# Performance work log

Hardware: AMD Instinct MI355X
Metric: run time of the kernel (lower is better)

The kernel has to match this reference:

```python
import jax, jax.numpy as jnp
import numpy as np

E, H, I = 8, 2048, 768  # num_experts, hidden_size, moe_intermediate_size
B, S = 4, 1024


def setup_inputs() -> dict:
    key = jax.random.key(0)
    k1, k2, k3, k4, k5 = jax.random.split(key, 5)
    hidden_states = jax.random.normal(k1, (B, S, H), dtype=jnp.float32)
    routing_weights = jax.random.uniform(k2, (B * S, E), dtype=jnp.float32)
    router_indices = jax.random.randint(k3, (B * S, 2), 0, E)
    gate_up_proj = jax.random.normal(k4, (E, H, 2 * I), dtype=jnp.float32) * 0.02
    down_proj = jax.random.normal(k5, (E, I, H), dtype=jnp.float32) * 0.02
    return {
        "hidden_states": hidden_states,
        "routing_weights": routing_weights,
        "router_indices": router_indices,
        "gate_up_proj": gate_up_proj,
        "down_proj": down_proj,
    }


def reference(hidden_states, routing_weights, router_indices, gate_up_proj, down_proj):
    b, s, h = hidden_states.shape
    x = hidden_states.reshape(-1, h)  # [T, H], T = B*S
    # dense all-experts: every token through every expert
    gate_up = jnp.einsum("th,ehd->etd", x, gate_up_proj)  # [E, T, 2I]
    gate, up = jnp.split(gate_up, 2, axis=-1)
    inter = up * jax.nn.silu(gate)  # [E, T, I]
    out = jnp.einsum("eti,eih->eth", inter, down_proj)  # [E, T, H]
    rw = routing_weights.T.reshape(out.shape[0], b, s)  # [E, B, S]
    out = out.reshape(out.shape[0], b, s, h) * rw[..., None]
    return out.sum(axis=0)  # [B, S, H]
```

## Files before the change

kernel.cpp:

```cpp
#include <hip/hip_runtime.h>
#include <cstdint>
#include <cstddef>

#define NE 8
#define NH 2048
#define NI 768
#define NT 4096
#define NK2 6144

typedef __bf16 bf16x8 __attribute__((ext_vector_type(8)));
typedef float f32x4 __attribute__((ext_vector_type(4)));
typedef unsigned short u16x8 __attribute__((ext_vector_type(8)));

__device__ __forceinline__ unsigned short f2bf(float f) {
  unsigned int u = __builtin_bit_cast(unsigned int, f);
  u += 0x7fffu + ((u >> 16) & 1u);
  return (unsigned short)(u >> 16);
}

__device__ __forceinline__ void gload_lds16(const void* g, void* s) {
  __builtin_amdgcn_global_load_lds(
      (const __attribute__((address_space(1))) unsigned int*)g,
      (__attribute__((address_space(3))) unsigned int*)s, 16, 0, 0);
}

__global__ __launch_bounds__(256) void k_cvt(const float* __restrict__ in,
                                             unsigned short* __restrict__ out,
                                             long n) {
  long i = ((long)blockIdx.x * blockDim.x + threadIdx.x) * 8;
  if (i >= n) return;
  float4 f0 = *reinterpret_cast<const float4*>(in + i);
  float4 f1 = *reinterpret_cast<const float4*>(in + i + 4);
  u16x8 o;
  o[0] = f2bf(f0.x); o[1] = f2bf(f0.y); o[2] = f2bf(f0.z); o[3] = f2bf(f0.w);
  o[4] = f2bf(f1.x); o[5] = f2bf(f1.y); o[6] = f2bf(f1.z); o[7] = f2bf(f1.w);
  *reinterpret_cast<u16x8*>(out + i) = o;
}

__global__ __launch_bounds__(256) void k_transpose_cvt(
    const float* __restrict__ in, unsigned short* __restrict__ out,
    int R, int C, long inBS, long outBS, int outCS, int mode) {
  __shared__ float tile[32][33];
  const int b = blockIdx.z;
  const int r0 = blockIdx.y * 32, c0 = blockIdx.x * 32;
  const int tx = threadIdx.x, ty = threadIdx.y;
  const float* ib = in + (long)b * inBS;
#pragma unroll
  for (int d = 0; d < 4; d++)
    tile[ty + d * 8][tx] = ib[(long)(r0 + ty + d * 8) * C + c0 + tx];
  __syncthreads();
#pragma unroll
  for (int d = 0; d < 4; d++) {
    int c = c0 + ty + d * 8;
    int r = r0 + tx;
    int orow;
    if (mode == 1) {
      int z = (c >= NI) ? 1 : 0;
      int cc = c - z * NI;
      orow = ((cc >> 4) << 5) + (z << 4) + (cc & 15);
    } else {
      orow = c;
    }
    out[(long)b * outBS + (long)orow * outCS + r] = f2bf(tile[tx][ty + d * 8]);
  }
}


__global__ __launch_bounds__(512, 1) void k_gemm1(
    const unsigned short* __restrict__ Xb,
    const unsigned short* __restrict__ W1t,
    const float* __restrict__ rw,
    unsigned short* __restrict__ inter) {
  __shared__ unsigned short ldsA[2][16384];
  __shared__ unsigned short ldsB[2][16384];

  const int e = blockIdx.z;
  const int t0 = blockIdx.y * 256;
  const int bn = blockIdx.x;
  const int tid = threadIdx.x;
  const int lane = tid & 63, wave = tid >> 6;
  const int wr = wave >> 2, wc = wave & 3;
  const int fr = lane & 15, fq = lane >> 4;
  const int nkt = NH / 64;

  const unsigned short* Bg = W1t + (size_t)e * (2 * NI) * NH;
  const int rih = tid >> 3, ck = tid & 7;
  const unsigned short* sA = Xb + (size_t)(t0 + rih) * NH + ((ck ^ (rih & 7)) << 3);
  const unsigned short* sB = Bg + (size_t)(bn * 256 + rih) * NH + ((ck ^ (rih & 7)) << 3);
  const int dst = tid * 8;

#define STG_H0(C) do { \
    const int cc_ = (C); const size_t ko_ = (size_t)cc_ * 64; \
    unsigned short* da_ = &ldsA[cc_ & 1][dst]; \
    unsigned short* db_ = &ldsB[cc_ & 1][dst]; \
    gload_lds16(sB + ko_, db_); \
    gload_lds16(sB + ko_ + (size_t)(64 * NH), db_ + 4096); \
    gload_lds16(sA + ko_, da_); \
    gload_lds16(sA + ko_ + (size_t)(64 * NH), da_ + 4096); \
  } while (0)
#define STG_H1(C) do { \
    const int cc_ = (C); const size_t ko_ = (size_t)cc_ * 64; \
    unsigned short* da_ = &ldsA[cc_ & 1][dst]; \
    unsigned short* db_ = &ldsB[cc_ & 1][dst]; \
    gload_lds16(sB + ko_ + (size_t)2 * (64 * NH), db_ + 8192); \
    gload_lds16(sB + ko_ + (size_t)3 * (64 * NH), db_ + 12288); \
    gload_lds16(sA + ko_ + (size_t)2 * (64 * NH), da_ + 8192); \
    gload_lds16(sA + ko_ + (size_t)3 * (64 * NH), da_ + 12288); \
  } while (0)
#define WAITV4 asm volatile("s_waitcnt vmcnt(4)" ::: "memory")
#define BAR do { __builtin_amdgcn_sched_barrier(0); \
                 __builtin_amdgcn_s_barrier(); \
                 __builtin_amdgcn_sched_barrier(0); } while (0)

  f32x4 acc[8][4];
#pragma unroll
  for (int i = 0; i < 8; ++i)
#pragma unroll
    for (int j = 0; j < 4; ++j) acc[i][j] = (f32x4){0.f, 0.f, 0.f, 0.f};

  const int swz = fr & 7;
  int aoff[8], boff[4];
#pragma unroll
  for (int i = 0; i < 8; ++i)
    aoff[i] = ((i >> 2) * 128 + wr * 64 + (i & 3) * 16 + fr) * 64 + ((fq ^ swz) << 3);
#pragma unroll
  for (int j = 0; j < 4; ++j)
    boff[j] = ((j >> 1) * 128 + wc * 32 + (j & 1) * 16 + fr) * 64 + ((fq ^ swz) << 3);
  const int dk = ((((4 + fq) ^ swz) - (fq ^ swz)) << 3);

  STG_H0(0);
  STG_H1(0);
  WAITV4;
  BAR;

  for (int kt = 0; kt < nkt; ++kt) {
    const int cur = kt & 1;
    const int nx = (kt + 1 < nkt) ? kt + 1 : nkt - 1;
    const unsigned short* lA = ldsA[cur];
    const unsigned short* lB = ldsB[cur];
    bf16x8 af0[4][2], af1[4][2], bf0[2][2], bf1[2][2];

#pragma unroll
    for (int m = 0; m < 4; ++m) {
      af0[m][0] = *reinterpret_cast<const bf16x8*>(lA + aoff[m]);
      af0[m][1] = *reinterpret_cast<const bf16x8*>(lA + aoff[m] + dk);
    }
#pragma unroll
    for (int jj = 0; jj < 2; ++jj) {
      bf0[jj][0] = *reinterpret_cast<const bf16x8*>(lB + boff[jj]);
      bf0[jj][1] = *reinterpret_cast<const bf16x8*>(lB + boff[jj] + dk);
    }
    STG_H0(nx);
    WAITV4;
    BAR;
    __builtin_amdgcn_s_setprio(1);
#pragma unroll
    for (int kk = 0; kk < 2; ++kk)
#pragma unroll
      for (int m = 0; m < 4; ++m)
#pragma unroll
        for (int jj = 0; jj < 2; ++jj)
          acc[m][jj] = __builtin_amdgcn_mfma_f32_16x16x32_bf16(af0[m][kk], bf0[jj][kk], acc[m][jj], 0, 0, 0);
    __builtin_amdgcn_s_setprio(0);

#pragma unroll
    for (int jj = 0; jj < 2; ++jj) {
      bf1[jj][0] = *reinterpret_cast<const bf16x8*>(lB + boff[2 + jj]);
      bf1[jj][1] = *reinterpret_cast<const bf16x8*>(lB + boff[2 + jj] + dk);
    }
    STG_H1(nx);
    BAR;
    __builtin_amdgcn_s_setprio(1);
#pragma unroll
    for (int kk = 0; kk < 2; ++kk)
#pragma unroll
      for (int m = 0; m < 4; ++m)
#pragma unroll
        for (int jj = 0; jj < 2; ++jj)
          acc[m][2 + jj] = __builtin_amdgcn_mfma_f32_16x16x32_bf16(af0[m][kk], bf1[jj][kk], acc[m][2 + jj], 0, 0, 0);
    __builtin_amdgcn_s_setprio(0);

#pragma unroll
    for (int m = 0; m < 4; ++m) {
      af1[m][0] = *reinterpret_cast<const bf16x8*>(lA + aoff[4 + m]);
      af1[m][1] = *reinterpret_cast<const bf16x8*>(lA + aoff[4 + m] + dk);
    }
    BAR;
    __builtin_amdgcn_s_setprio(1);
#pragma unroll
    for (int kk = 0; kk < 2; ++kk)
#pragma unroll
      for (int m = 0; m < 4; ++m)
#pragma unroll
        for (int jj = 0; jj < 2; ++jj)
          acc[4 + m][2 + jj] = __builtin_amdgcn_mfma_f32_16x16x32_bf16(af1[m][kk], bf1[jj][kk], acc[4 + m][2 + jj], 0, 0, 0);
    __builtin_amdgcn_s_setprio(0);

#pragma unroll
    for (int jj = 0; jj < 2; ++jj) {
      bf0[jj][0] = *reinterpret_cast<const bf16x8*>(lB + boff[jj]);
      bf0[jj][1] = *reinterpret_cast<const bf16x8*>(lB + boff[jj] + dk);
    }
    WAITV4;
    BAR;
    __builtin_amdgcn_s_setprio(1);
#pragma unroll
    for (int kk = 0; kk < 2; ++kk)
#pragma unroll
      for (int m = 0; m < 4; ++m)
#pragma unroll
        for (int jj = 0; jj < 2; ++jj)
          acc[4 + m][jj] = __builtin_amdgcn_mfma_f32_16x16x32_bf16(af1[m][kk], bf0[jj][kk], acc[4 + m][jj], 0, 0, 0);
    __builtin_amdgcn_s_setprio(0);
  }
  asm volatile("s_waitcnt vmcnt(0)" ::: "memory");
#undef STG_H0
#undef STG_H1
#undef WAITV4
#undef BAR

#pragma unroll
  for (int i = 0; i < 8; ++i) {
    const int trow = t0 + (i >> 2) * 128 + wr * 64 + (i & 3) * 16 + fq * 4;
#pragma unroll
    for (int r = 0; r < 4; ++r) {
      const int t = trow + r;
      const float rwv = rw[(size_t)t * NE + e];
#pragma unroll
      for (int p = 0; p < 2; ++p) {
        float g = acc[i][2 * p][r];
        float u = acc[i][2 * p + 1][r];
        float s = g / (1.f + __expf(-g));
        const int col = bn * 128 + (p * 4 + wc) * 16 + fr;
        inter[(size_t)t * NK2 + e * NI + col] = f2bf(rwv * u * s);
      }
    }
  }
}

__global__ __launch_bounds__(512, 2) void k_gemm2(
    const unsigned short* __restrict__ inter,
    const unsigned short* __restrict__ W2t,
    float* __restrict__ out) {
  __shared__ unsigned short ldsA[2][16384];
  __shared__ unsigned short ldsB[2][8192];

  const int t0 = blockIdx.y * 256;
  const int h0 = blockIdx.x * 128;
  const int tid = threadIdx.x;
  const int lane = tid & 63, wave = tid >> 6;
  const int wr = wave >> 1, wc = wave & 1;
  const int fr = lane & 15, fq = lane >> 4;
  const int nkt = NK2 / 64;

  const int rih = tid >> 3, ck = tid & 7;
  const unsigned short* sA = inter + (size_t)(t0 + rih) * NK2 + ((ck ^ (rih & 7)) << 3);
  const unsigned short* sB = W2t + (size_t)(h0 + rih) * NK2 + ((ck ^ (rih & 7)) << 3);
  const int dst = tid * 8;

#define STG2(C) do { \
    const int cc_ = (C); \
    unsigned short* da_ = &ldsA[cc_ & 1][dst]; \
    unsigned short* db_ = &ldsB[cc_ & 1][dst]; \
    const size_t ko_ = (size_t)cc_ * 64; \
    _Pragma("unroll") \
    for (int q = 0; q < 4; ++q) \
      gload_lds16(sA + ko_ + (size_t)q * (64 * NK2), da_ + q * 4096); \
    _Pragma("unroll") \
    for (int q = 0; q < 2; ++q) \
      gload_lds16(sB + ko_ + (size_t)q * (64 * NK2), db_ + q * 4096); \
  } while (0)

  f32x4 acc[4][4];
#pragma unroll
  for (int i = 0; i < 4; ++i)
#pragma unroll
    for (int j = 0; j < 4; ++j) acc[i][j] = (f32x4){0.f, 0.f, 0.f, 0.f};

  const int swz = fr & 7;
  int aoff[4], boff[4];
#pragma unroll
  for (int i = 0; i < 4; ++i)
    aoff[i] = (wr * 64 + i * 16 + fr) * 64 + ((fq ^ swz) << 3);
#pragma unroll
  for (int j = 0; j < 4; ++j)
    boff[j] = (wc * 64 + j * 16 + fr) * 64 + ((fq ^ swz) << 3);
  const int dk = ((((4 + fq) ^ swz) - (fq ^ swz)) << 3);

  STG2(0);
  STG2(1);

  for (int kt = 0; kt < nkt; ++kt) {
    const int cur = kt & 1;
    const int nx = (kt + 1 < nkt) ? kt + 1 : nkt - 1;
    STG2(nx);
    asm volatile("s_waitcnt vmcnt(6)" ::: "memory");
    __builtin_amdgcn_sched_barrier(0);
    __builtin_amdgcn_s_barrier();
    __builtin_amdgcn_sched_barrier(0);
    {
      bf16x8 af[4], bf[4];
#pragma unroll
      for (int i = 0; i < 4; ++i)
        af[i] = *reinterpret_cast<const bf16x8*>(&ldsA[cur][aoff[i]]);
#pragma unroll
      for (int j = 0; j < 4; ++j)
        bf[j] = *reinterpret_cast<const bf16x8*>(&ldsB[cur][boff[j]]);
      __builtin_amdgcn_s_setprio(1);
#pragma unroll
      for (int i = 0; i < 4; ++i)
#pragma unroll
        for (int j = 0; j < 4; ++j)
          acc[i][j] = __builtin_amdgcn_mfma_f32_16x16x32_bf16(af[i], bf[j], acc[i][j], 0, 0, 0);
      __builtin_amdgcn_s_setprio(0);
    }
    {
      bf16x8 af[4], bf[4];
#pragma unroll
      for (int i = 0; i < 4; ++i)
        af[i] = *reinterpret_cast<const bf16x8*>(&ldsA[cur][aoff[i] + dk]);
#pragma unroll
      for (int j = 0; j < 4; ++j)
        bf[j] = *reinterpret_cast<const bf16x8*>(&ldsB[cur][boff[j] + dk]);
      __builtin_amdgcn_sched_barrier(0);
      __builtin_amdgcn_s_barrier();
      __builtin_amdgcn_sched_barrier(0);
      __builtin_amdgcn_s_setprio(1);
#pragma unroll
      for (int i = 0; i < 4; ++i)
#pragma unroll
        for (int j = 0; j < 4; ++j)
          acc[i][j] = __builtin_amdgcn_mfma_f32_16x16x32_bf16(af[i], bf[j], acc[i][j], 0, 0, 0);
      __builtin_amdgcn_s_setprio(0);
    }
  }
  asm volatile("s_waitcnt vmcnt(0)" ::: "memory");
#undef STG2

  const int rowBase = t0 + wr * 64 + fq * 4;
#pragma unroll
  for (int i = 0; i < 4; ++i)
#pragma unroll
    for (int j = 0; j < 4; ++j)
#pragma unroll
      for (int r = 0; r < 4; ++r)
        out[(size_t)(rowBase + i * 16 + r) * NH + h0 + wc * 64 + j * 16 + fr] =
            acc[i][j][r];
}

extern "C" void kernel_launch(void* const* d_in, const int* in_sizes, int n_in,
                              void* d_out, int out_size, void* d_ws, size_t ws_size,
                              hipStream_t stream) {
  const float* x = (const float*)d_in[0];
  const float* rw = (const float*)d_in[1];
  const float* w1 = (const float*)d_in[3];
  const float* w2 = (const float*)d_in[4];
  float* out = (float*)d_out;

  char* ws = (char*)d_ws;
  unsigned short* Xb = (unsigned short*)ws;
  unsigned short* W1t = (unsigned short*)(ws + 16777216);
  unsigned short* W2t = (unsigned short*)(ws + 16777216 + 50331648);
  unsigned short* inter = (unsigned short*)(ws + 16777216 + 50331648 + 25165824);

  k_cvt<<<dim3((NT * NH) / (256 * 8)), dim3(256), 0, stream>>>(x, Xb, (long)NT * NH);
  k_transpose_cvt<<<dim3((2 * NI) / 32, NH / 32, NE), dim3(32, 8), 0, stream>>>(
      w1, W1t, NH, 2 * NI, (long)NH * 2 * NI, (long)2 * NI * NH, NH, 1);
  k_transpose_cvt<<<dim3(NH / 32, NI / 32, NE), dim3(32, 8), 0, stream>>>(
      w2, W2t, NI, NH, (long)NI * NH, (long)NI, NK2, 0);
  k_gemm1<<<dim3((2 * NI) / 256, NT / 256, NE), dim3(512), 0, stream>>>(Xb, W1t, rw, inter);
  k_gemm2<<<dim3(NH / 128, NT / 256), dim3(512), 0, stream>>>(inter, W2t, out);
}
```

Measured before the change: 366.7 us.

## Deepen the GEMM1 LDS prefetch to two tiles ahead with per-quarter buffer reuse

The monolithic half-tile staging macros are split into per-quarter A and B loads. The next tile's remaining quarters and three quarters of tile kt+2 are issued into LDS regions of the current buffer as soon as those regions have been consumed. The wait is relaxed to vmcnt(10) so more global-to-LDS loads stay in flight behind the MFMA phases. The redundant reload of the bf0 fragments before the last MFMA phase is dropped, since they are still in registers. The gain in latency hiding depends on the barriers ordering every overwrite after all waves have read that region, so a scheduling slip would corrupt data.

```diff
diff --git a/kernel.cpp b/kernel.cpp
--- a/kernel.cpp
+++ b/kernel.cpp
@@ -89,25 +89,20 @@
   const unsigned short* sB = Bg + (size_t)(bn * 256 + rih) * NH + ((ck ^ (rih & 7)) << 3);
   const int dst = tid * 8;
 
-#define STG_H0(C) do { \
-    const int cc_ = (C); const size_t ko_ = (size_t)cc_ * 64; \
-    unsigned short* da_ = &ldsA[cc_ & 1][dst]; \
-    unsigned short* db_ = &ldsB[cc_ & 1][dst]; \
-    gload_lds16(sB + ko_, db_); \
-    gload_lds16(sB + ko_ + (size_t)(64 * NH), db_ + 4096); \
-    gload_lds16(sA + ko_, da_); \
-    gload_lds16(sA + ko_ + (size_t)(64 * NH), da_ + 4096); \
-  } while (0)
-#define STG_H1(C) do { \
-    const int cc_ = (C); const size_t ko_ = (size_t)cc_ * 64; \
-    unsigned short* da_ = &ldsA[cc_ & 1][dst]; \
-    unsigned short* db_ = &ldsB[cc_ & 1][dst]; \
-    gload_lds16(sB + ko_ + (size_t)2 * (64 * NH), db_ + 8192); \
-    gload_lds16(sB + ko_ + (size_t)3 * (64 * NH), db_ + 12288); \
-    gload_lds16(sA + ko_ + (size_t)2 * (64 * NH), da_ + 8192); \
-    gload_lds16(sA + ko_ + (size_t)3 * (64 * NH), da_ + 12288); \
-  } while (0)
-#define WAITV4 asm volatile("s_waitcnt vmcnt(4)" ::: "memory")
+#define SRC_K(TT) ((size_t)(((TT) < nkt) ? (TT) : (nkt - 1)) * 64)
+#define SU_A0(TT) do { unsigned short* L_ = ldsA[(TT) & 1]; const size_t k_ = SRC_K(TT); \
+    gload_lds16(sA + k_,                       L_ + dst); \
+    gload_lds16(sA + k_ + (size_t)64 * NH,     L_ + dst + 4096); } while (0)
+#define SU_A1(TT) do { unsigned short* L_ = ldsA[(TT) & 1]; const size_t k_ = SRC_K(TT); \
+    gload_lds16(sA + k_ + (size_t)128 * NH,    L_ + dst + 8192); \
+    gload_lds16(sA + k_ + (size_t)192 * NH,    L_ + dst + 12288); } while (0)
+#define SU_B0(TT) do { unsigned short* L_ = ldsB[(TT) & 1]; const size_t k_ = SRC_K(TT); \
+    gload_lds16(sB + k_,                       L_ + dst); \
+    gload_lds16(sB + k_ + (size_t)64 * NH,     L_ + dst + 4096); } while (0)
+#define SU_B1(TT) do { unsigned short* L_ = ldsB[(TT) & 1]; const size_t k_ = SRC_K(TT); \
+    gload_lds16(sB + k_ + (size_t)128 * NH,    L_ + dst + 8192); \
+    gload_lds16(sB + k_ + (size_t)192 * NH,    L_ + dst + 12288); } while (0)
+#define WAITV10 asm volatile("s_waitcnt vmcnt(10)" ::: "memory")
 #define BAR do { __builtin_amdgcn_sched_barrier(0); \
                  __builtin_amdgcn_s_barrier(); \
                  __builtin_amdgcn_sched_barrier(0); } while (0)
@@ -128,14 +123,12 @@
     boff[j] = ((j >> 1) * 128 + wc * 32 + (j & 1) * 16 + fr) * 64 + ((fq ^ swz) << 3);
   const int dk = ((((4 + fq) ^ swz) - (fq ^ swz)) << 3);
 
-  STG_H0(0);
-  STG_H1(0);
-  WAITV4;
+  SU_A0(0); SU_B0(0); SU_B1(0); SU_A1(0); SU_A0(1); SU_B0(1); SU_B1(1);
+  WAITV10;
   BAR;
 
   for (int kt = 0; kt < nkt; ++kt) {
     const int cur = kt & 1;
-    const int nx = (kt + 1 < nkt) ? kt + 1 : nkt - 1;
     const unsigned short* lA = ldsA[cur];
     const unsigned short* lB = ldsB[cur];
     bf16x8 af0[4][2], af1[4][2], bf0[2][2], bf1[2][2];
@@ -150,8 +143,8 @@
       bf0[jj][0] = *reinterpret_cast<const bf16x8*>(lB + boff[jj]);
       bf0[jj][1] = *reinterpret_cast<const bf16x8*>(lB + boff[jj] + dk);
     }
-    STG_H0(nx);
-    WAITV4;
+    SU_A1(kt + 1);
+    WAITV10;
     BAR;
     __builtin_amdgcn_s_setprio(1);
 #pragma unroll
@@ -168,7 +161,8 @@
       bf1[jj][0] = *reinterpret_cast<const bf16x8*>(lB + boff[2 + jj]);
       bf1[jj][1] = *reinterpret_cast<const bf16x8*>(lB + boff[2 + jj] + dk);
     }
-    STG_H1(nx);
+    SU_A0(kt + 2);
+    WAITV10;
     BAR;
     __builtin_amdgcn_s_setprio(1);
 #pragma unroll
@@ -185,6 +179,7 @@
       af1[m][0] = *reinterpret_cast<const bf16x8*>(lA + aoff[4 + m]);
       af1[m][1] = *reinterpret_cast<const bf16x8*>(lA + aoff[4 + m] + dk);
     }
+    SU_B0(kt + 2);
     BAR;
     __builtin_amdgcn_s_setprio(1);
 #pragma unroll
@@ -196,12 +191,8 @@
           acc[4 + m][2 + jj] = __builtin_amdgcn_mfma_f32_16x16x32_bf16(af1[m][kk], bf1[jj][kk], acc[4 + m][2 + jj], 0, 0, 0);
     __builtin_amdgcn_s_setprio(0);
 
-#pragma unroll
-    for (int jj = 0; jj < 2; ++jj) {
-      bf0[jj][0] = *reinterpret_cast<const bf16x8*>(lB + boff[jj]);
-      bf0[jj][1] = *reinterpret_cast<const bf16x8*>(lB + boff[jj] + dk);
-    }
-    WAITV4;
+    SU_B1(kt + 2);
+    WAITV10;
     BAR;
     __builtin_amdgcn_s_setprio(1);
 #pragma unroll
@@ -214,9 +205,12 @@
     __builtin_amdgcn_s_setprio(0);
   }
   asm volatile("s_waitcnt vmcnt(0)" ::: "memory");
-#undef STG_H0
-#undef STG_H1
-#undef WAITV4
+#undef SRC_K
+#undef SU_A0
+#undef SU_A1
+#undef SU_B0
+#undef SU_B1
+#undef WAITV10
 #undef BAR
 
 #pragma unroll
```

After: 371.3 us. Within noise of the previous version (+1.2%).
